# Kernel optimization log

Hardware: AMD Instinct MI355X
Metric: run time of the kernel (lower is better)

Reference implementation:

```python
import jax, jax.numpy as jnp
import numpy as np
import math

PHI = (1.0 + math.sqrt(5.0)) / 2.0
LN_EPS = 1e-5


def _carrier_phases(n_heads: int) -> np.ndarray:
    """Reproduce DimensionalHeadManager._allocate carrier phases."""
    base = [k * math.pi / 7.0 for k in range(7)]  # rung base phases
    n_rungs = 7
    raw = []
    remaining = n_heads
    for i in range(n_rungs):
        if i < n_rungs - 1:
            c = max(1, round(n_heads / PHI ** (i + 1)))
            c = min(c, remaining - (n_rungs - 1 - i))
            raw.append(c)
            remaining -= c
        else:
            raw.append(max(1, remaining))
    phases = []
    for rung_idx, count in enumerate(raw):
        for j in range(count):
            phases.append(base[rung_idx] + 2.0 * math.pi / max(count, 1) * j)
    return np.asarray(phases[:n_heads], dtype=np.float32)


def setup_inputs() -> dict:
    key = jax.random.key(0)
    ks = jax.random.split(key, 7)
    B, S, D, H = 2, 2048, 1024, 16
    w_scale = 0.02  # realistic init scale for Linear weights
    x = jax.random.normal(ks[0], (B, S, D), dtype=jnp.float32)
    Wq = jax.random.normal(ks[1], (D, D), dtype=jnp.float32) * w_scale
    Wk = jax.random.normal(ks[2], (D, D), dtype=jnp.float32) * w_scale
    Wv = jax.random.normal(ks[3], (D, D), dtype=jnp.float32) * w_scale
    Wo = jax.random.normal(ks[4], (D, D), dtype=jnp.float32) * w_scale
    Wp = jax.random.normal(ks[5], (D,), dtype=jnp.float32) * w_scale  # W_phase (1,D) flattened
    gamma = jnp.ones((D,), dtype=jnp.float32)
    beta = jnp.zeros((D,), dtype=jnp.float32)
    carrier = jnp.asarray(_carrier_phases(H))  # srl.carrier_freq init
    lam = jnp.float32(0.1)  # lambda_resonance init
    return {"x": x, "Wq": Wq, "Wk": Wk, "Wv": Wv, "Wo": Wo, "Wp": Wp,
            "gamma": gamma, "beta": beta, "carrier": carrier, "lam": lam}


def reference(x, Wq, Wk, Wv, Wo, Wp, gamma, beta, carrier, lam):
    B, S, D = x.shape
    H = carrier.shape[0]
    dh = D // H
    scale = 1.0 / math.sqrt(dh)

    residual = x
    # LayerNorm
    mu = jnp.mean(x, axis=-1, keepdims=True)
    var = jnp.mean((x - mu) ** 2, axis=-1, keepdims=True)
    xn = (x - mu) * jax.lax.rsqrt(var + LN_EPS) * gamma + beta

    # Q/K/V projections (torch Linear: y = x @ W.T), split into heads
    q = jnp.einsum('bsd,ed->bse', xn, Wq).reshape(B, S, H, dh)
    k = jnp.einsum('bsd,ed->bse', xn, Wk).reshape(B, S, H, dh)
    v = jnp.einsum('bsd,ed->bse', xn, Wv).reshape(B, S, H, dh)

    # scalar phase per token, per-head carrier resonance gate
    phase = jnp.einsum('bsd,d->bs', xn, Wp)                       # (B,S)
    head_T = jnp.cos((phase[..., None] - carrier) * 0.5) ** 2     # (B,S,H)

    # attention scores + resonance term R_ij = cos^2((phi_i - phi_j)/2)
    scores = jnp.einsum('bihd,bjhd->bhij', q, k) * scale          # (B,H,S,S)
    R = jnp.cos((phase[:, :, None] - phase[:, None, :]) * 0.5) ** 2  # (B,S,S)
    scores = scores + lam * R[:, None, :, :]

    attn = jax.nn.softmax(scores, axis=-1)
    out = jnp.einsum('bhij,bjhd->bihd', attn, v)                  # (B,S,H,dh)
    out = out * head_T[..., None]                                 # per-head resonance gating
    emergent_energy = jnp.sum(jnp.abs(out))
    y = residual + jnp.einsum('bse,de->bsd', out.reshape(B, S, D), Wo)
    return (y, emergent_energy)
```

## Files before the change

kernel.cpp:

```cpp
#include <hip/hip_runtime.h>
#include <hip/hip_bf16.h>

#define S_LEN 2048
#define D_MODEL 1024
#define NH 16
#define DH 64
#define M_TOK 4096
#define DK 80

typedef __attribute__((ext_vector_type(8))) short bf16x8;
typedef __attribute__((ext_vector_type(4))) float f32x4;
typedef __attribute__((ext_vector_type(16))) float f32x16;

#define LOG2E 1.4426950408889634f

__device__ __forceinline__ unsigned short f2bf(float f) {
  unsigned u = __float_as_uint(f);
  u += 0x7FFF + ((u >> 16) & 1);
  return (unsigned short)(u >> 16);
}

__device__ __forceinline__ void gl16(const void* g, void* l) {
  __builtin_amdgcn_global_load_lds(
      (const __attribute__((address_space(1))) unsigned int*)g,
      (__attribute__((address_space(3))) unsigned int*)l, 16, 0, 0);
}

__global__ __launch_bounds__(256) void prep_kernel(
    const float* __restrict__ Wq, const float* __restrict__ Wk,
    const float* __restrict__ Wv, const float* __restrict__ Wo,
    unsigned short* __restrict__ wbf, float* __restrict__ energy) {
  if (blockIdx.x == 0 && threadIdx.x == 0) *energy = 0.f;
  int idx = (blockIdx.x * 256 + threadIdx.x) * 4;
  int wsel = idx >> 20;
  const float* s = (wsel == 0) ? Wq : (wsel == 1) ? Wk : (wsel == 2) ? Wv : Wo;
  int off = idx & 1048575;
  float4 v = *(const float4*)(s + off);
  ushort4 p;
  p.x = f2bf(v.x); p.y = f2bf(v.y); p.z = f2bf(v.z); p.w = f2bf(v.w);
  *(ushort4*)(wbf + idx) = p;
}

__device__ __forceinline__ float block_sum(float v, float* sm) {
#pragma unroll
  for (int o = 32; o > 0; o >>= 1) v += __shfl_xor(v, o, 64);
  int w = threadIdx.x >> 6;
  __syncthreads();
  if ((threadIdx.x & 63) == 0) sm[w] = v;
  __syncthreads();
  return sm[0] + sm[1] + sm[2] + sm[3];
}

__global__ __launch_bounds__(256) void ln_phase_kernel(
    const float* __restrict__ x, const float* __restrict__ Wp,
    const float* __restrict__ gamma, const float* __restrict__ beta,
    unsigned short* __restrict__ xn, float* __restrict__ cosP,
    float* __restrict__ sinP) {
  __shared__ float sm[4];
  int row = blockIdx.x;
  int tid = threadIdx.x;
  float4 v = ((const float4*)(x + (size_t)row * D_MODEL))[tid];
  float mu = block_sum(v.x + v.y + v.z + v.w, sm) * (1.0f / D_MODEL);
  float d0 = v.x - mu, d1 = v.y - mu, d2 = v.z - mu, d3 = v.w - mu;
  float var = block_sum(d0 * d0 + d1 * d1 + d2 * d2 + d3 * d3, sm) * (1.0f / D_MODEL);
  float rinv = rsqrtf(var + 1e-5f);
  float4 g = ((const float4*)gamma)[tid];
  float4 be = ((const float4*)beta)[tid];
  float n0 = d0 * rinv * g.x + be.x;
  float n1 = d1 * rinv * g.y + be.y;
  float n2 = d2 * rinv * g.z + be.z;
  float n3 = d3 * rinv * g.w + be.w;
  ushort4 p;
  p.x = f2bf(n0); p.y = f2bf(n1); p.z = f2bf(n2); p.w = f2bf(n3);
  ((ushort4*)(xn + (size_t)row * D_MODEL))[tid] = p;
  float4 wp = ((const float4*)Wp)[tid];
  float ph = block_sum(n0 * wp.x + n1 * wp.y + n2 * wp.z + n3 * wp.w, sm);
  if (tid == 0) {
    cosP[row] = cosf(ph);
    sinP[row] = sinf(ph);
  }
}

__global__ __launch_bounds__(256) void phase_fill_kernel(
    const float* __restrict__ cosP, const float* __restrict__ sinP,
    unsigned short* __restrict__ kk80) {
  int gid = blockIdx.x * 256 + threadIdx.x;
  int s = gid & (S_LEN - 1);
  int bh = gid >> 11;
  int b = bh >> 4;
  int tok = b * S_LEN + s;
  unsigned int w0 = (unsigned int)f2bf(cosP[tok]) | ((unsigned int)f2bf(sinP[tok]) << 16);
  int4 lo = make_int4((int)w0, 0, 0, 0);
  int4 hi = make_int4(0, 0, 0, 0);
  *(int4*)(kk80 + (size_t)gid * DK + 64) = lo;
  *(int4*)(kk80 + (size_t)gid * DK + 72) = hi;
}

__global__ __launch_bounds__(256) void qkv_gemm_kernel(
    const unsigned short* __restrict__ xn, const unsigned short* __restrict__ wbf,
    unsigned short* __restrict__ q, unsigned short* __restrict__ kk80,
    unsigned short* __restrict__ vT) {
  __shared__ __align__(16) unsigned short As[128 * 64];
  __shared__ __align__(16) unsigned short Bs[128 * 64];
  int z = blockIdx.z;
  const unsigned short* Wm = wbf + (size_t)z * (D_MODEL * D_MODEL);
  const unsigned short* Ap = (z == 2) ? Wm : xn;
  const unsigned short* Bp = (z == 2) ? xn : Wm;
  int m0 = (z == 2) ? blockIdx.x * 128 : blockIdx.y * 128;
  int n0 = (z == 2) ? blockIdx.y * 128 : blockIdx.x * 128;
  int tid = threadIdx.x;
  int wave = tid >> 6, lane = tid & 63, quad = lane >> 4, l15 = lane & 15;
  int wm = (wave & 1) * 64, wn = (wave >> 1) * 64;
  f32x4 acc[4][4];
#pragma unroll
  for (int r = 0; r < 4; ++r)
#pragma unroll
    for (int c = 0; c < 4; ++c) acc[r][c] = (f32x4){0.f, 0.f, 0.f, 0.f};

  for (int k0 = 0; k0 < D_MODEL; k0 += 64) {
    __syncthreads();
#pragma unroll
    for (int t = 0; t < 4; ++t) {
      int c = t * 256 + tid;
      int r = c >> 3, p = c & 7;
      int qc = p ^ (r & 7);
      gl16(&Ap[(size_t)(m0 + r) * D_MODEL + k0 + qc * 8], &As[c * 8]);
      gl16(&Bp[(size_t)(n0 + r) * D_MODEL + k0 + qc * 8], &Bs[c * 8]);
    }
    __syncthreads();
    bf16x8 af[4][2], bfr[4][2];
#pragma unroll
    for (int r = 0; r < 4; ++r) {
      int R = wm + r * 16 + l15;
#pragma unroll
      for (int h = 0; h < 2; ++h)
        af[r][h] = *(const bf16x8*)&As[R * 64 + ((h * 4 + quad) ^ (R & 7)) * 8];
    }
#pragma unroll
    for (int c = 0; c < 4; ++c) {
      int R = wn + c * 16 + l15;
#pragma unroll
      for (int h = 0; h < 2; ++h)
        bfr[c][h] = *(const bf16x8*)&Bs[R * 64 + ((h * 4 + quad) ^ (R & 7)) * 8];
    }
#pragma unroll
    for (int h = 0; h < 2; ++h)
#pragma unroll
      for (int r = 0; r < 4; ++r)
#pragma unroll
        for (int c = 0; c < 4; ++c)
          acc[r][c] = __builtin_amdgcn_mfma_f32_16x16x32_bf16(af[r][h], bfr[c][h], acc[r][c], 0, 0, 0);
  }
#pragma unroll
  for (int r = 0; r < 4; ++r) {
#pragma unroll
    for (int c = 0; c < 4; ++c) {
#pragma unroll
      for (int rr = 0; rr < 4; ++rr) {
        if (z == 2) {
          int e = m0 + wm + r * 16 + quad * 4 + rr;
          int tok = n0 + wn + c * 16 + l15;
          int hh = e >> 6, d = e & 63;
          int bb = tok >> 11, ss = tok & (S_LEN - 1);
          vT[(((size_t)(bb * NH + hh)) * DH + d) * S_LEN + ss] = f2bf(acc[r][c][rr]);
        } else {
          int tok = m0 + wm + r * 16 + quad * 4 + rr;
          int e = n0 + wn + c * 16 + l15;
          int hh = e >> 6, d = e & 63;
          int bb = tok >> 11, ss = tok & (S_LEN - 1);
          if (z == 0) {
            unsigned short val = f2bf(acc[r][c][rr] * (0.125f * LOG2E));
            q[(((size_t)(bb * NH + hh)) * S_LEN + ss) * DH + d] = val;
          } else {
            kk80[(((size_t)(bb * NH + hh)) * S_LEN + ss) * DK + d] = f2bf(acc[r][c][rr]);
          }
        }
      }
    }
  }
}

__global__ __launch_bounds__(256) void attn_kernel(
    const unsigned short* __restrict__ q, const unsigned short* __restrict__ kk80,
    const unsigned short* __restrict__ vT, const float* __restrict__ cosP,
    const float* __restrict__ sinP, const float* __restrict__ carrier,
    const float* __restrict__ lamp, unsigned short* __restrict__ outw,
    float* __restrict__ energy) {
  __shared__ __align__(16) unsigned short Ks[640 * 8];
  __shared__ __align__(16) unsigned short Vs[512 * 8];
  __shared__ __align__(16) unsigned int Ps[4][32 * 34];
  __shared__ float Lr[4][32];
  __shared__ float er[4];
  int qt = blockIdx.x, h = blockIdx.y, b = blockIdx.z;
  int bh = b * NH + h;
  int tid = threadIdx.x, wave = tid >> 6, lane = tid & 63;
  int half = lane >> 5, l31 = lane & 31;

  const unsigned short* kb = kk80 + (size_t)bh * S_LEN * DK;
  const unsigned short* vb = vT + (size_t)bh * DH * S_LEN;
  int qrow = qt * 128 + wave * 32 + l31;

  bf16x8 bQ[5];
  {
    const unsigned short* qp = q + ((size_t)bh * S_LEN + qrow) * DH;
#pragma unroll
    for (int db = 0; db < 4; ++db)
      bQ[db] = *(const bf16x8*)(qp + db * 16 + half * 8);
    bf16x8 z8 = {0, 0, 0, 0, 0, 0, 0, 0};
    if (half == 0) {
      float hl2 = 0.5f * lamp[0] * LOG2E;
      z8[0] = (short)f2bf(hl2 * cosP[b * S_LEN + qrow]);
      z8[1] = (short)f2bf(hl2 * sinP[b * S_LEN + qrow]);
    }
    bQ[4] = z8;
  }

  f32x16 O0 = {}, O1 = {};
  float l_i = 0.f;

  for (int j0 = 0; j0 < S_LEN; j0 += 64) {
    __syncthreads();
#pragma unroll
    for (int t = 0; t < 2; ++t) {
      int cc = t * 256 + tid;
      int r = (cc * 205) >> 11;
      int p = cc - r * 10;
      int g = p + ((r >> 2) & 3);
      if (g >= 10) g -= 10;
      gl16(&kb[(size_t)(j0 + r) * DK + g * 8], (unsigned short*)Ks + cc * 8);
    }
    if (tid < 128) {
      int cc = 512 + tid;
      int r = (cc * 205) >> 11;
      int p = cc - r * 10;
      int g = p + ((r >> 2) & 3);
      if (g >= 10) g -= 10;
      gl16(&kb[(size_t)(j0 + r) * DK + g * 8], (unsigned short*)Ks + cc * 8);
    }
#pragma unroll
    for (int t = 0; t < 2; ++t) {
      int cc = t * 256 + tid;
      int r = cc >> 3, p = cc & 7;
      int g = p ^ (r & 7);
      gl16(&vb[(size_t)r * S_LEN + j0 + g * 8], (unsigned short*)Vs + cc * 8);
    }
    __syncthreads();

    f32x16 Sf[2];
#pragma unroll
    for (int sj = 0; sj < 2; ++sj) {
      Sf[sj] = (f32x16){};
      int r = sj * 32 + l31;
      int rot = (r >> 2) & 3;
#pragma unroll
      for (int db = 0; db < 5; ++db) {
        int p = db * 2 + half - rot;
        if (p < 0) p += 10;
        bf16x8 aK = *(const bf16x8*)((const unsigned short*)Ks + (r * 10 + p) * 8);
        Sf[sj] = __builtin_amdgcn_mfma_f32_32x32x16_bf16(aK, bQ[db], Sf[sj], 0, 0, 0);
      }
    }

#pragma unroll
    for (int sj = 0; sj < 2; ++sj) {
#pragma unroll
      for (int rr = 0; rr < 8; ++rr) {
        float e0 = exp2f(Sf[sj][rr * 2 + 0]);
        float e1 = exp2f(Sf[sj][rr * 2 + 1]);
        l_i += e0 + e1;
        __hip_bfloat162 pk = __float22bfloat162_rn(float2{e0, e1});
        int jd = sj * 16 + (rr >> 1) * 4 + half * 2 + (rr & 1);
        Ps[wave][l31 * 34 + jd] = *(unsigned int*)&pk;
      }
    }

#pragma unroll
    for (int jb = 0; jb < 4; ++jb) {
      const unsigned int* pp = &Ps[wave][l31 * 34 + jb * 8 + half * 4];
      uint2 a0 = *(const uint2*)pp;
      uint2 a1 = *(const uint2*)(pp + 2);
      union { unsigned int u[4]; bf16x8 v; } cvt;
      cvt.u[0] = a0.x; cvt.u[1] = a0.y; cvt.u[2] = a1.x; cvt.u[3] = a1.y;
      {
        int rv = l31;
        int p = (jb * 2 + half) ^ (rv & 7);
        bf16x8 bV = *(const bf16x8*)((const unsigned short*)Vs + (rv * 8 + p) * 8);
        O0 = __builtin_amdgcn_mfma_f32_32x32x16_bf16(cvt.v, bV, O0, 0, 0, 0);
      }
      {
        int rv = 32 + l31;
        int p = (jb * 2 + half) ^ (rv & 7);
        bf16x8 bV = *(const bf16x8*)((const unsigned short*)Vs + (rv * 8 + p) * 8);
        O1 = __builtin_amdgcn_mfma_f32_32x32x16_bf16(cvt.v, bV, O1, 0, 0, 0);
      }
    }
  }

  l_i += __shfl_xor(l_i, 32, 64);
  Lr[wave][l31] = l_i;
  float ch = cosf(carrier[h]), sh = sinf(carrier[h]);
  float esum = 0.f;
#pragma unroll
  for (int reg = 0; reg < 16; ++reg) {
    int ir = (reg & 3) + 8 * (reg >> 2) + 4 * half;
    int srow = qt * 128 + wave * 32 + ir;
    float cp = cosP[b * S_LEN + srow], sp = sinP[b * S_LEN + srow];
    float gate = 0.5f + 0.5f * (cp * ch + sp * sh);
    float gl = gate / Lr[wave][ir];
    size_t tok = (size_t)b * S_LEN + srow;
    float v0 = O0[reg] * gl, v1 = O1[reg] * gl;
    esum += fabsf(v0) + fabsf(v1);
    outw[tok * D_MODEL + h * DH + l31] = f2bf(v0);
    outw[tok * D_MODEL + h * DH + 32 + l31] = f2bf(v1);
  }
#pragma unroll
  for (int off = 32; off > 0; off >>= 1) esum += __shfl_xor(esum, off, 64);
  if (lane == 0) er[wave] = esum;
  __syncthreads();
  if (tid == 0) atomicAdd(energy, er[0] + er[1] + er[2] + er[3]);
}

__global__ __launch_bounds__(256) void out_gemm_kernel(
    const unsigned short* __restrict__ A, const unsigned short* __restrict__ Wo,
    const float* __restrict__ x, float* __restrict__ y) {
  __shared__ __align__(16) unsigned short As[128 * 64];
  __shared__ __align__(16) unsigned short Bs[128 * 64];
  int tid = threadIdx.x;
  int wave = tid >> 6, lane = tid & 63, quad = lane >> 4, l15 = lane & 15;
  int wm = (wave & 1) * 64, wn = (wave >> 1) * 64;
  int m0 = blockIdx.y * 128, n0 = blockIdx.x * 128;
  f32x4 acc[4][4];
#pragma unroll
  for (int r = 0; r < 4; ++r)
#pragma unroll
    for (int c = 0; c < 4; ++c) acc[r][c] = (f32x4){0.f, 0.f, 0.f, 0.f};

  for (int k0 = 0; k0 < D_MODEL; k0 += 64) {
    __syncthreads();
#pragma unroll
    for (int t = 0; t < 4; ++t) {
      int c = t * 256 + tid;
      int r = c >> 3, p = c & 7;
      int qc = p ^ (r & 7);
      gl16(&A[(size_t)(m0 + r) * D_MODEL + k0 + qc * 8], &As[c * 8]);
      gl16(&Wo[(size_t)(n0 + r) * D_MODEL + k0 + qc * 8], &Bs[c * 8]);
    }
    __syncthreads();
    bf16x8 af[4][2], bfr[4][2];
#pragma unroll
    for (int r = 0; r < 4; ++r) {
      int R = wm + r * 16 + l15;
#pragma unroll
      for (int h = 0; h < 2; ++h)
        af[r][h] = *(const bf16x8*)&As[R * 64 + ((h * 4 + quad) ^ (R & 7)) * 8];
    }
#pragma unroll
    for (int c = 0; c < 4; ++c) {
      int R = wn + c * 16 + l15;
#pragma unroll
      for (int h = 0; h < 2; ++h)
        bfr[c][h] = *(const bf16x8*)&Bs[R * 64 + ((h * 4 + quad) ^ (R & 7)) * 8];
    }
#pragma unroll
    for (int h = 0; h < 2; ++h)
#pragma unroll
      for (int r = 0; r < 4; ++r)
#pragma unroll
        for (int c = 0; c < 4; ++c)
          acc[r][c] = __builtin_amdgcn_mfma_f32_16x16x32_bf16(af[r][h], bfr[c][h], acc[r][c], 0, 0, 0);
  }
#pragma unroll
  for (int r = 0; r < 4; ++r) {
#pragma unroll
    for (int c = 0; c < 4; ++c) {
      int dcol = n0 + wn + c * 16 + l15;
#pragma unroll
      for (int rr = 0; rr < 4; ++rr) {
        int tok = m0 + wm + r * 16 + quad * 4 + rr;
        size_t idx = (size_t)tok * D_MODEL + dcol;
        y[idx] = x[idx] + acc[r][c][rr];
      }
    }
  }
}

extern "C" void kernel_launch(void* const* d_in, const int* in_sizes, int n_in,
                              void* d_out, int out_size, void* d_ws, size_t ws_size,
                              hipStream_t stream) {
  const float* x = (const float*)d_in[0];
  const float* Wq = (const float*)d_in[1];
  const float* Wk = (const float*)d_in[2];
  const float* Wv = (const float*)d_in[3];
  const float* Wo = (const float*)d_in[4];
  const float* Wp = (const float*)d_in[5];
  const float* gamma = (const float*)d_in[6];
  const float* beta = (const float*)d_in[7];
  const float* carrier = (const float*)d_in[8];
  const float* lam = (const float*)d_in[9];

  char* ws = (char*)d_ws;
  const size_t MB = 1024 * 1024;
  unsigned short* wbf = (unsigned short*)(ws);
  unsigned short* xn = (unsigned short*)(ws + 8 * MB);
  unsigned short* qq = (unsigned short*)(ws + 16 * MB);
  unsigned short* kk80 = (unsigned short*)(ws + 24 * MB);
  unsigned short* vT = (unsigned short*)(ws + 34 * MB);
  float* cosP = (float*)(ws + 42 * MB);
  float* sinP = (float*)(ws + 42 * MB + 16 * 1024);
  unsigned short* outw = xn;

  float* y = (float*)d_out;
  float* energy = y + (out_size - 1);

  prep_kernel<<<4096, 256, 0, stream>>>(Wq, Wk, Wv, Wo, wbf, energy);
  ln_phase_kernel<<<M_TOK, 256, 0, stream>>>(x, Wp, gamma, beta, xn, cosP, sinP);
  phase_fill_kernel<<<256, 256, 0, stream>>>(cosP, sinP, kk80);
  qkv_gemm_kernel<<<dim3(8, 32, 3), 256, 0, stream>>>(xn, wbf, qq, kk80, vT);
  attn_kernel<<<dim3(16, 16, 2), 256, 0, stream>>>(qq, kk80, vT, cosP, sinP,
                                                   carrier, lam, outw, energy);
  out_gemm_kernel<<<dim3(8, 32), 256, 0, stream>>>(outw, wbf + 3 * D_MODEL * D_MODEL,
                                                   x, y);
}
```

Before: 242.6 us.

## Split attention KV range across two wave groups and halve GEMM N-tiles

The attention kernel now launches 512 threads per block. Two groups of four waves each process half of the key sequence with their own K/V shared-memory buffers, then the partial outputs and row sums are combined through shared memory before gating and writing. The QKV and output GEMMs use 128x64 tiles instead of 128x128, which doubles the block count. The aim is more parallelism and occupancy on a 256-CU GPU, since before the change attention had only 512 blocks. The cost is an extra combine step, more shared memory per attention block, and less operand reuse in the GEMMs.

```diff
diff --git a/kernel.cpp b/kernel.cpp
--- a/kernel.cpp
+++ b/kernel.cpp
@@ -101,21 +101,22 @@
     unsigned short* __restrict__ q, unsigned short* __restrict__ kk80,
     unsigned short* __restrict__ vT) {
   __shared__ __align__(16) unsigned short As[128 * 64];
-  __shared__ __align__(16) unsigned short Bs[128 * 64];
+  __shared__ __align__(16) unsigned short Bs[64 * 64];
   int z = blockIdx.z;
   const unsigned short* Wm = wbf + (size_t)z * (D_MODEL * D_MODEL);
   const unsigned short* Ap = (z == 2) ? Wm : xn;
   const unsigned short* Bp = (z == 2) ? xn : Wm;
-  int m0 = (z == 2) ? blockIdx.x * 128 : blockIdx.y * 128;
-  int n0 = (z == 2) ? blockIdx.y * 128 : blockIdx.x * 128;
+  int bx = blockIdx.x, by = blockIdx.y;
+  int m0 = (z == 2) ? (bx >> 1) * 128 : by * 128;
+  int n0 = (z == 2) ? (by * 2 + (bx & 1)) * 64 : bx * 64;
   int tid = threadIdx.x;
   int wave = tid >> 6, lane = tid & 63, quad = lane >> 4, l15 = lane & 15;
-  int wm = (wave & 1) * 64, wn = (wave >> 1) * 64;
-  f32x4 acc[4][4];
+  int wm = (wave & 1) * 64, wn = (wave >> 1) * 32;
+  f32x4 acc[4][2];
 #pragma unroll
   for (int r = 0; r < 4; ++r)
 #pragma unroll
-    for (int c = 0; c < 4; ++c) acc[r][c] = (f32x4){0.f, 0.f, 0.f, 0.f};
+    for (int c = 0; c < 2; ++c) acc[r][c] = (f32x4){0.f, 0.f, 0.f, 0.f};
 
   for (int k0 = 0; k0 < D_MODEL; k0 += 64) {
     __syncthreads();
@@ -125,10 +126,16 @@
       int r = c >> 3, p = c & 7;
       int qc = p ^ (r & 7);
       gl16(&Ap[(size_t)(m0 + r) * D_MODEL + k0 + qc * 8], &As[c * 8]);
+    }
+#pragma unroll
+    for (int t = 0; t < 2; ++t) {
+      int c = t * 256 + tid;
+      int r = c >> 3, p = c & 7;
+      int qc = p ^ (r & 7);
       gl16(&Bp[(size_t)(n0 + r) * D_MODEL + k0 + qc * 8], &Bs[c * 8]);
     }
     __syncthreads();
-    bf16x8 af[4][2], bfr[4][2];
+    bf16x8 af[4][2], bfr[2][2];
 #pragma unroll
     for (int r = 0; r < 4; ++r) {
       int R = wm + r * 16 + l15;
@@ -137,7 +144,7 @@
         af[r][h] = *(const bf16x8*)&As[R * 64 + ((h * 4 + quad) ^ (R & 7)) * 8];
     }
 #pragma unroll
-    for (int c = 0; c < 4; ++c) {
+    for (int c = 0; c < 2; ++c) {
       int R = wn + c * 16 + l15;
 #pragma unroll
       for (int h = 0; h < 2; ++h)
@@ -148,13 +155,13 @@
 #pragma unroll
       for (int r = 0; r < 4; ++r)
 #pragma unroll
-        for (int c = 0; c < 4; ++c)
+        for (int c = 0; c < 2; ++c)
           acc[r][c] = __builtin_amdgcn_mfma_f32_16x16x32_bf16(af[r][h], bfr[c][h], acc[r][c], 0, 0, 0);
   }
 #pragma unroll
   for (int r = 0; r < 4; ++r) {
 #pragma unroll
-    for (int c = 0; c < 4; ++c) {
+    for (int c = 0; c < 2; ++c) {
 #pragma unroll
       for (int rr = 0; rr < 4; ++rr) {
         if (z == 2) {
@@ -180,25 +187,27 @@
   }
 }
 
-__global__ __launch_bounds__(256) void attn_kernel(
+__global__ __launch_bounds__(512) void attn_kernel(
     const unsigned short* __restrict__ q, const unsigned short* __restrict__ kk80,
     const unsigned short* __restrict__ vT, const float* __restrict__ cosP,
     const float* __restrict__ sinP, const float* __restrict__ carrier,
     const float* __restrict__ lamp, unsigned short* __restrict__ outw,
     float* __restrict__ energy) {
-  __shared__ __align__(16) unsigned short Ks[640 * 8];
-  __shared__ __align__(16) unsigned short Vs[512 * 8];
-  __shared__ __align__(16) unsigned int Ps[4][32 * 34];
-  __shared__ float Lr[4][32];
+  __shared__ __align__(16) unsigned short Ks[2][640 * 8];
+  __shared__ __align__(16) unsigned short Vs[2][512 * 8];
+  __shared__ __align__(16) unsigned int Ps[8][32 * 34];
+  __shared__ float Lr[8][32];
   __shared__ float er[4];
   int qt = blockIdx.x, h = blockIdx.y, b = blockIdx.z;
   int bh = b * NH + h;
   int tid = threadIdx.x, wave = tid >> 6, lane = tid & 63;
   int half = lane >> 5, l31 = lane & 31;
+  int grp = wave >> 2, wq = wave & 3;
+  int tid2 = tid & 255;
 
   const unsigned short* kb = kk80 + (size_t)bh * S_LEN * DK;
   const unsigned short* vb = vT + (size_t)bh * DH * S_LEN;
-  int qrow = qt * 128 + wave * 32 + l31;
+  int qrow = qt * 128 + wq * 32 + l31;
 
   bf16x8 bQ[5];
   {
@@ -218,31 +227,34 @@
   f32x16 O0 = {}, O1 = {};
   float l_i = 0.f;
 
-  for (int j0 = 0; j0 < S_LEN; j0 += 64) {
-    __syncthreads();
+  for (int j0 = 0; j0 < S_LEN / 2; j0 += 64) {
+    int jbase = grp * (S_LEN / 2) + j0;
+    __syncthreads();
+    unsigned short* Ksg = &Ks[grp][0];
+    unsigned short* Vsg = &Vs[grp][0];
 #pragma unroll
     for (int t = 0; t < 2; ++t) {
-      int cc = t * 256 + tid;
+      int cc = t * 256 + tid2;
       int r = (cc * 205) >> 11;
       int p = cc - r * 10;
       int g = p + ((r >> 2) & 3);
       if (g >= 10) g -= 10;
-      gl16(&kb[(size_t)(j0 + r) * DK + g * 8], (unsigned short*)Ks + cc * 8);
-    }
-    if (tid < 128) {
-      int cc = 512 + tid;
+      gl16(&kb[(size_t)(jbase + r) * DK + g * 8], Ksg + cc * 8);
+    }
+    if (tid2 < 128) {
+      int cc = 512 + tid2;
       int r = (cc * 205) >> 11;
       int p = cc - r * 10;
       int g = p + ((r >> 2) & 3);
       if (g >= 10) g -= 10;
-      gl16(&kb[(size_t)(j0 + r) * DK + g * 8], (unsigned short*)Ks + cc * 8);
+      gl16(&kb[(size_t)(jbase + r) * DK + g * 8], Ksg + cc * 8);
     }
 #pragma unroll
     for (int t = 0; t < 2; ++t) {
-      int cc = t * 256 + tid;
+      int cc = t * 256 + tid2;
       int r = cc >> 3, p = cc & 7;
       int g = p ^ (r & 7);
-      gl16(&vb[(size_t)r * S_LEN + j0 + g * 8], (unsigned short*)Vs + cc * 8);
+      gl16(&vb[(size_t)r * S_LEN + jbase + g * 8], Vsg + cc * 8);
     }
     __syncthreads();
 
@@ -256,7 +268,7 @@
       for (int db = 0; db < 5; ++db) {
         int p = db * 2 + half - rot;
         if (p < 0) p += 10;
-        bf16x8 aK = *(const bf16x8*)((const unsigned short*)Ks + (r * 10 + p) * 8);
+        bf16x8 aK = *(const bf16x8*)(Ksg + (r * 10 + p) * 8);
         Sf[sj] = __builtin_amdgcn_mfma_f32_32x32x16_bf16(aK, bQ[db], Sf[sj], 0, 0, 0);
       }
     }
@@ -284,38 +296,54 @@
       {
         int rv = l31;
         int p = (jb * 2 + half) ^ (rv & 7);
-        bf16x8 bV = *(const bf16x8*)((const unsigned short*)Vs + (rv * 8 + p) * 8);
+        bf16x8 bV = *(const bf16x8*)(Vsg + (rv * 8 + p) * 8);
         O0 = __builtin_amdgcn_mfma_f32_32x32x16_bf16(cvt.v, bV, O0, 0, 0, 0);
       }
       {
         int rv = 32 + l31;
         int p = (jb * 2 + half) ^ (rv & 7);
-        bf16x8 bV = *(const bf16x8*)((const unsigned short*)Vs + (rv * 8 + p) * 8);
+        bf16x8 bV = *(const bf16x8*)(Vsg + (rv * 8 + p) * 8);
         O1 = __builtin_amdgcn_mfma_f32_32x32x16_bf16(cvt.v, bV, O1, 0, 0, 0);
       }
     }
   }
 
+  __syncthreads();
   l_i += __shfl_xor(l_i, 32, 64);
   Lr[wave][l31] = l_i;
-  float ch = cosf(carrier[h]), sh = sinf(carrier[h]);
+  float* Om = (float*)&Ps[0][0];
+  if (grp == 1) {
+#pragma unroll
+    for (int reg = 0; reg < 16; ++reg) {
+      int ir = (reg & 3) + 8 * (reg >> 2) + 4 * half;
+      Om[wq * 2048 + ir * 64 + l31] = O0[reg];
+      Om[wq * 2048 + ir * 64 + 32 + l31] = O1[reg];
+    }
+  }
+  __syncthreads();
   float esum = 0.f;
-#pragma unroll
-  for (int reg = 0; reg < 16; ++reg) {
-    int ir = (reg & 3) + 8 * (reg >> 2) + 4 * half;
-    int srow = qt * 128 + wave * 32 + ir;
-    float cp = cosP[b * S_LEN + srow], sp = sinP[b * S_LEN + srow];
-    float gate = 0.5f + 0.5f * (cp * ch + sp * sh);
-    float gl = gate / Lr[wave][ir];
-    size_t tok = (size_t)b * S_LEN + srow;
-    float v0 = O0[reg] * gl, v1 = O1[reg] * gl;
-    esum += fabsf(v0) + fabsf(v1);
-    outw[tok * D_MODEL + h * DH + l31] = f2bf(v0);
-    outw[tok * D_MODEL + h * DH + 32 + l31] = f2bf(v1);
+  if (grp == 0) {
+    float ch = cosf(carrier[h]), sh = sinf(carrier[h]);
+#pragma unroll
+    for (int reg = 0; reg < 16; ++reg) {
+      int ir = (reg & 3) + 8 * (reg >> 2) + 4 * half;
+      int srow = qt * 128 + wq * 32 + ir;
+      float v0 = O0[reg] + Om[wq * 2048 + ir * 64 + l31];
+      float v1 = O1[reg] + Om[wq * 2048 + ir * 64 + 32 + l31];
+      float lt = Lr[wq][ir] + Lr[wq + 4][ir];
+      float cp = cosP[b * S_LEN + srow], sp = sinP[b * S_LEN + srow];
+      float gate = 0.5f + 0.5f * (cp * ch + sp * sh);
+      float gl = gate / lt;
+      v0 *= gl; v1 *= gl;
+      esum += fabsf(v0) + fabsf(v1);
+      size_t tok = (size_t)b * S_LEN + srow;
+      outw[tok * D_MODEL + h * DH + l31] = f2bf(v0);
+      outw[tok * D_MODEL + h * DH + 32 + l31] = f2bf(v1);
+    }
   }
 #pragma unroll
   for (int off = 32; off > 0; off >>= 1) esum += __shfl_xor(esum, off, 64);
-  if (lane == 0) er[wave] = esum;
+  if (lane == 0 && grp == 0) er[wave] = esum;
   __syncthreads();
   if (tid == 0) atomicAdd(energy, er[0] + er[1] + er[2] + er[3]);
 }
@@ -324,16 +352,16 @@
     const unsigned short* __restrict__ A, const unsigned short* __restrict__ Wo,
     const float* __restrict__ x, float* __restrict__ y) {
   __shared__ __align__(16) unsigned short As[128 * 64];
-  __shared__ __align__(16) unsigned short Bs[128 * 64];
+  __shared__ __align__(16) unsigned short Bs[64 * 64];
   int tid = threadIdx.x;
   int wave = tid >> 6, lane = tid & 63, quad = lane >> 4, l15 = lane & 15;
-  int wm = (wave & 1) * 64, wn = (wave >> 1) * 64;
-  int m0 = blockIdx.y * 128, n0 = blockIdx.x * 128;
-  f32x4 acc[4][4];
+  int wm = (wave & 1) * 64, wn = (wave >> 1) * 32;
+  int m0 = blockIdx.y * 128, n0 = blockIdx.x * 64;
+  f32x4 acc[4][2];
 #pragma unroll
   for (int r = 0; r < 4; ++r)
 #pragma unroll
-    for (int c = 0; c < 4; ++c) acc[r][c] = (f32x4){0.f, 0.f, 0.f, 0.f};
+    for (int c = 0; c < 2; ++c) acc[r][c] = (f32x4){0.f, 0.f, 0.f, 0.f};
 
   for (int k0 = 0; k0 < D_MODEL; k0 += 64) {
     __syncthreads();
@@ -343,10 +371,16 @@
       int r = c >> 3, p = c & 7;
       int qc = p ^ (r & 7);
       gl16(&A[(size_t)(m0 + r) * D_MODEL + k0 + qc * 8], &As[c * 8]);
+    }
+#pragma unroll
+    for (int t = 0; t < 2; ++t) {
+      int c = t * 256 + tid;
+      int r = c >> 3, p = c & 7;
+      int qc = p ^ (r & 7);
       gl16(&Wo[(size_t)(n0 + r) * D_MODEL + k0 + qc * 8], &Bs[c * 8]);
     }
     __syncthreads();
-    bf16x8 af[4][2], bfr[4][2];
+    bf16x8 af[4][2], bfr[2][2];
 #pragma unroll
     for (int r = 0; r < 4; ++r) {
       int R = wm + r * 16 + l15;
@@ -355,7 +389,7 @@
         af[r][h] = *(const bf16x8*)&As[R * 64 + ((h * 4 + quad) ^ (R & 7)) * 8];
     }
 #pragma unroll
-    for (int c = 0; c < 4; ++c) {
+    for (int c = 0; c < 2; ++c) {
       int R = wn + c * 16 + l15;
 #pragma unroll
       for (int h = 0; h < 2; ++h)
@@ -366,13 +400,13 @@
 #pragma unroll
       for (int r = 0; r < 4; ++r)
 #pragma unroll
-        for (int c = 0; c < 4; ++c)
+        for (int c = 0; c < 2; ++c)
           acc[r][c] = __builtin_amdgcn_mfma_f32_16x16x32_bf16(af[r][h], bfr[c][h], acc[r][c], 0, 0, 0);
   }
 #pragma unroll
   for (int r = 0; r < 4; ++r) {
 #pragma unroll
-    for (int c = 0; c < 4; ++c) {
+    for (int c = 0; c < 2; ++c) {
       int dcol = n0 + wn + c * 16 + l15;
 #pragma unroll
       for (int rr = 0; rr < 4; ++rr) {
@@ -415,9 +449,9 @@
   prep_kernel<<<4096, 256, 0, stream>>>(Wq, Wk, Wv, Wo, wbf, energy);
   ln_phase_kernel<<<M_TOK, 256, 0, stream>>>(x, Wp, gamma, beta, xn, cosP, sinP);
   phase_fill_kernel<<<256, 256, 0, stream>>>(cosP, sinP, kk80);
-  qkv_gemm_kernel<<<dim3(8, 32, 3), 256, 0, stream>>>(xn, wbf, qq, kk80, vT);
-  attn_kernel<<<dim3(16, 16, 2), 256, 0, stream>>>(qq, kk80, vT, cosP, sinP,
+  qkv_gemm_kernel<<<dim3(16, 32, 3), 256, 0, stream>>>(xn, wbf, qq, kk80, vT);
+  attn_kernel<<<dim3(16, 16, 2), 512, 0, stream>>>(qq, kk80, vT, cosP, sinP,
                                                    carrier, lam, outw, energy);
-  out_gemm_kernel<<<dim3(8, 32), 256, 0, stream>>>(outw, wbf + 3 * D_MODEL * D_MODEL,
-                                                   x, y);
-}
+  out_gemm_kernel<<<dim3(16, 32), 256, 0, stream>>>(outw, wbf + 3 * D_MODEL * D_MODEL,
+                                                    x, y);
+}
```

Result: faster. 230.9 us (-4.8%).
